# Optimization experiments

Measured on AMD Instinct MI355X. Metric: run time of the kernel, lower is better.

The kernel has to match this reference:

```python
import jax, jax.numpy as jnp
import numpy as np

N_NODES = 50000
N_EDGES = 800000
IN_FEATS = 128
H_FEATS = 128
NUM_CLASSES = 64


def _linear_params(key, fan_in, fan_out):
    kw, kb = jax.random.split(key)
    bound = 1.0 / np.sqrt(fan_in)
    W = jax.random.uniform(kw, (fan_out, fan_in), minval=-bound, maxval=bound, dtype=jnp.float32)
    b = jax.random.uniform(kb, (fan_out,), minval=-bound, maxval=bound, dtype=jnp.float32)
    return W, b


def setup_inputs() -> dict:
    key = jax.random.key(0)
    k_feat, k_src, k_dst, k1, k2, k3 = jax.random.split(key, 6)
    in_feat = jax.random.normal(k_feat, (N_NODES, IN_FEATS), dtype=jnp.float32)
    src = jax.random.randint(k_src, (N_EDGES,), 0, N_NODES, dtype=jnp.int32)
    dst = jax.random.randint(k_dst, (N_EDGES,), 0, N_NODES, dtype=jnp.int32)
    W1, b1 = _linear_params(k1, IN_FEATS, H_FEATS)
    W2, b2 = _linear_params(k2, H_FEATS, H_FEATS)
    W3, b3 = _linear_params(k3, H_FEATS, NUM_CLASSES)
    return {"in_feat": in_feat, "W1": W1, "b1": b1, "W2": W2, "b2": b2,
            "W3": W3, "b3": b3, "src": src, "dst": dst}


def reference(in_feat, W1, b1, W2, b2, W3, b3, src, dst):
    N = in_feat.shape[0]

    def gin_layer(x, W, b):
        # DGL GINConv with eps=0: (x + sum of in-neighbor messages) -> Linear
        agg = jax.ops.segment_sum(x[src], dst, num_segments=N)  # [N, d]
        return jax.nn.relu((x + agg) @ W.T + b)

    h = gin_layer(in_feat, W1, b1)
    h = gin_layer(h, W2, b2)
    h = gin_layer(h, W3, b3)
    return h
```

## Files before the change

kernel.cpp:

```cpp
#include <hip/hip_runtime.h>

typedef _Float16 half8 __attribute__((ext_vector_type(8)));
typedef _Float16 half2v __attribute__((ext_vector_type(2)));
typedef float floatx4 __attribute__((ext_vector_type(4)));
typedef unsigned int uintx4 __attribute__((ext_vector_type(4)));

union AB { uint4 u; half8 h; };
union H2 { unsigned int u; _Float16 h[2]; };
union H2P { unsigned int u; half2v h; };

#define CAPLOG 6
#define CAP 64

__global__ __launch_bounds__(256) void histA_init_k(
    const int* __restrict__ dst, int* __restrict__ histG, int E, int nbins,
    const float* __restrict__ W1, const float* __restrict__ W2, const float* __restrict__ W3,
    _Float16* __restrict__ W1h, _Float16* __restrict__ W2h, _Float16* __restrict__ W3h,
    _Float16* __restrict__ z1, _Float16* __restrict__ h1, _Float16* __restrict__ hZ,
    int n4w1, int n4w2, int n4w3, int zoff128, int zoff64) {
    int t = threadIdx.x;
    if (blockIdx.x < 256) {
        __shared__ int h[256];
        h[t] = 0;
        __syncthreads();
        int per = (E + 255) / 256;
        int beg = blockIdx.x * per;
        int end = min(E, beg + per);
        for (int e = beg + t; e < end; e += 256)
            atomicAdd(&h[dst[e] >> 8], 1);
        __syncthreads();
        for (int i = t; i < nbins; i += 256)
            histG[i * 256 + blockIdx.x] = h[i];
        return;
    }
    int i = (blockIdx.x - 256) * 256 + t;
    const float* X;
    _Float16* O;
    int j;
    if (i < n4w1) { X = W1; O = W1h; j = i; }
    else if (i < n4w1 + n4w2) { X = W2; O = W2h; j = i - n4w1; }
    else if (i < n4w1 + n4w2 + n4w3) { X = W3; O = W3h; j = i - n4w1 - n4w2; }
    else {
        int z = i - (n4w1 + n4w2 + n4w3);
        if (z < 16) ((uint4*)z1)[zoff128 + z] = make_uint4(0, 0, 0, 0);
        else if (z < 32) ((uint4*)h1)[zoff128 + (z - 16)] = make_uint4(0, 0, 0, 0);
        else if (z < 40) ((uint4*)hZ)[zoff64 + (z - 32)] = make_uint4(0, 0, 0, 0);
        return;
    }
    float4 v = reinterpret_cast<const float4*>(X)[j];
    union { uint2 u; _Float16 h[4]; } o;
    o.h[0] = (_Float16)v.x; o.h[1] = (_Float16)v.y;
    o.h[2] = (_Float16)v.z; o.h[3] = (_Float16)v.w;
    reinterpret_cast<uint2*>(O)[j] = o.u;
}

__global__ __launch_bounds__(1024) void scan1_k(const int* __restrict__ x,
                                                int* __restrict__ inc,
                                                int* __restrict__ partial, int n) {
    __shared__ int sd[1024];
    int t = threadIdx.x;
    int v = blockIdx.x * 1024 + t;
    sd[t] = (v < n) ? x[v] : 0;
    __syncthreads();
    for (int off = 1; off < 1024; off <<= 1) {
        int val = (t >= off) ? sd[t - off] : 0;
        __syncthreads();
        sd[t] += val;
        __syncthreads();
    }
    if (v < n) inc[v] = sd[t];
    if (t == 1023) partial[blockIdx.x] = sd[1023];
}

__global__ __launch_bounds__(256) void scatterB_k(const int* __restrict__ src,
                                                  const int* __restrict__ dst,
                                                  const int* __restrict__ inc,
                                                  const int* __restrict__ histG,
                                                  const int* __restrict__ partial, int nparts,
                                                  unsigned int* __restrict__ binned,
                                                  int E, int nbins) {
    __shared__ int cur[256];
    __shared__ int pp[64];
    int t = threadIdx.x, blk = blockIdx.x;
    if (t < 64) {
        int v = (t < nparts) ? partial[t] : 0;
        for (int off = 1; off < 64; off <<= 1) {
            int n = __shfl_up(v, off, 64);
            if (t >= off) v += n;
        }
        int ex = __shfl_up(v, 1, 64);
        if (t == 0) ex = 0;
        pp[t] = ex;
    }
    __syncthreads();
    for (int i = t; i < nbins; i += 256) {
        int idx = i * 256 + blk;
        cur[i] = inc[idx] + pp[idx >> 10] - histG[idx];
    }
    __syncthreads();
    int per = (E + 255) / 256;
    int beg = blk * per;
    int end = min(E, beg + per);
    for (int e = beg + t; e < end; e += 256) {
        int d = dst[e];
        int s = src[e];
        int pos = atomicAdd(&cur[d >> 8], 1);
        binned[pos] = ((unsigned int)(d & 255) << 16) | (unsigned int)s;
    }
}

__global__ __launch_bounds__(256) void binB_k(const unsigned int* __restrict__ binned,
                                              const int* __restrict__ inc,
                                              const int* __restrict__ histG,
                                              const int* __restrict__ partial, int nparts,
                                              unsigned short* __restrict__ col,
                                              int* __restrict__ cnt,
                                              int N, int E, int nbins) {
    __shared__ unsigned short lcol[256 * CAP];
    __shared__ int lcnt[256];
    __shared__ int pp[64];
    __shared__ int bounds[2];
    int t = threadIdx.x;
    int b = blockIdx.x;
    if (t < 64) {
        int v = (t < nparts) ? partial[t] : 0;
        for (int off = 1; off < 64; off <<= 1) {
            int n = __shfl_up(v, off, 64);
            if (t >= off) v += n;
        }
        int ex = __shfl_up(v, 1, 64);
        if (t == 0) ex = 0;
        pp[t] = ex;
    }
    unsigned int* lcol32 = (unsigned int*)lcol;
    for (int i = t; i < 256 * CAP / 2; i += 256) lcol32[i] = 0xFFFFFFFFu;
    lcnt[t] = 0;
    __syncthreads();
    if (t == 0) {
        int i0 = b * 256;
        bounds[0] = inc[i0] + pp[i0 >> 10] - histG[i0];
    } else if (t == 1) {
        if (b == nbins - 1) bounds[1] = E;
        else {
            int i1 = (b + 1) * 256;
            bounds[1] = inc[i1] + pp[i1 >> 10] - histG[i1];
        }
    }
    __syncthreads();
    int beg = bounds[0], end = bounds[1];
    for (int e = beg + t; e < end; e += 256) {
        unsigned int u = binned[e];
        int dl = u >> 16;
        int pos = atomicAdd(&lcnt[dl], 1);
        if (pos < CAP)
            lcol[(dl << CAPLOG) + ((pos & 3) << 4) + (pos >> 2)] = (unsigned short)(u & 0xFFFFu);
    }
    __syncthreads();
    int base = b << 8;
    int nodes = min(256, N - base);
    uint4* colg = (uint4*)(col + ((size_t)base << CAPLOG));
    const uint4* coll = (const uint4*)lcol;
    for (int i = t; i < nodes * 8; i += 256) colg[i] = coll[i];
    for (int i = t; i < nodes; i += 256) cnt[base + i] = lcnt[i];
}

__global__ __launch_bounds__(256) void gemm_z1_k(const float* __restrict__ X,
                                                 const _Float16* __restrict__ Wh,
                                                 _Float16* __restrict__ z1, int nnodes) {
    constexpr int WSTR = 136;
    __shared__ _Float16 Wl[128 * WSTR];

    const int t = threadIdx.x;
    for (int p = t; p < 128 * 16; p += 256) {
        int f = p >> 4;
        int kq = (p & 15) * 8;
        *reinterpret_cast<uint4*>(&Wl[f * WSTR + kq]) =
            *reinterpret_cast<const uint4*>(Wh + f * 128 + kq);
    }
    __syncthreads();

    const int wave = t >> 6;
    const int lane = t & 63;
    const int quad = lane >> 4;
    const int fcol = lane & 15;
    const int m_base = (blockIdx.x * 4 + wave) * 16;
    const int row = m_base + fcol;
    const bool rowok = row < nnodes;

    floatx4 acc[8];
#pragma unroll
    for (int ft = 0; ft < 8; ft++) acc[ft] = (floatx4){0.f, 0.f, 0.f, 0.f};

    const float* Xrow = X + (size_t)row * 128;
#pragma unroll
    for (int step = 0; step < 4; step++) {
        AB a;
        if (rowok) {
            float4 f0 = *reinterpret_cast<const float4*>(Xrow + step * 32 + quad * 8);
            float4 f1 = *reinterpret_cast<const float4*>(Xrow + step * 32 + quad * 8 + 4);
            a.h[0] = (_Float16)f0.x; a.h[1] = (_Float16)f0.y;
            a.h[2] = (_Float16)f0.z; a.h[3] = (_Float16)f0.w;
            a.h[4] = (_Float16)f1.x; a.h[5] = (_Float16)f1.y;
            a.h[6] = (_Float16)f1.z; a.h[7] = (_Float16)f1.w;
        } else a.u = make_uint4(0u, 0u, 0u, 0u);
#pragma unroll
        for (int ft = 0; ft < 8; ft++) {
            half8 b = *reinterpret_cast<const half8*>(
                &Wl[(ft * 16 + fcol) * WSTR + step * 32 + quad * 8]);
            acc[ft] = __builtin_amdgcn_mfma_f32_16x16x32_f16(a.h, b, acc[ft], 0, 0, 0);
        }
    }

#pragma unroll
    for (int ft = 0; ft < 8; ft++) {
        int f = ft * 16 + fcol;
#pragma unroll
        for (int r = 0; r < 4; r++) {
            int node = m_base + quad * 4 + r;
            if (node < nnodes)
                z1[(size_t)node * 128 + f] = (_Float16)acc[ft][r];
        }
    }
}

__global__ __launch_bounds__(256) void agg128_k(const _Float16* __restrict__ Z,
                                                const int* __restrict__ cnt,
                                                const unsigned short* __restrict__ col,
                                                const float* __restrict__ bias,
                                                _Float16* __restrict__ H, int nnodes) {
    int w = blockIdx.x * 4 + (threadIdx.x >> 6);
    int lane = threadIdx.x & 63;
    if (w >= nnodes) return;
    const int q = lane >> 4;
    const int c15 = lane & 15;
    const unsigned int* X32 = reinterpret_cast<const unsigned int*>(Z);
    int deg = cnt[w];
    if (deg > CAP) deg = CAP;
    int nb = (deg + 15) >> 4;
    const unsigned short* c = col + ((size_t)w << CAPLOG) + (q << 4);

    H2P a0[4], a1[4], a2[4], a3[4];
#pragma unroll
    for (int m = 0; m < 4; m++) { a0[m].u = 0u; a1[m].u = 0u; a2[m].u = 0u; a3[m].u = 0u; }

    for (int t = 0; t < nb; t++) {
        uint2 iw = *reinterpret_cast<const uint2*>(c + t * 4);
        int s0 = (int)(iw.x & 0xFFFFu); s0 = (s0 < nnodes) ? s0 : nnodes;
        int s1 = (int)(iw.x >> 16);     s1 = (s1 < nnodes) ? s1 : nnodes;
        int s2 = (int)(iw.y & 0xFFFFu); s2 = (s2 < nnodes) ? s2 : nnodes;
        int s3 = (int)(iw.y >> 16);     s3 = (s3 < nnodes) ? s3 : nnodes;
        uint4 v0 = *reinterpret_cast<const uint4*>(X32 + (size_t)s0 * 64 + c15 * 4);
        uint4 v1 = *reinterpret_cast<const uint4*>(X32 + (size_t)s1 * 64 + c15 * 4);
        uint4 v2 = *reinterpret_cast<const uint4*>(X32 + (size_t)s2 * 64 + c15 * 4);
        uint4 v3 = *reinterpret_cast<const uint4*>(X32 + (size_t)s3 * 64 + c15 * 4);
        H2P u;
        u.u = v0.x; a0[0].h += u.h;  u.u = v0.y; a0[1].h += u.h;
        u.u = v0.z; a0[2].h += u.h;  u.u = v0.w; a0[3].h += u.h;
        u.u = v1.x; a1[0].h += u.h;  u.u = v1.y; a1[1].h += u.h;
        u.u = v1.z; a1[2].h += u.h;  u.u = v1.w; a1[3].h += u.h;
        u.u = v2.x; a2[0].h += u.h;  u.u = v2.y; a2[1].h += u.h;
        u.u = v2.z; a2[2].h += u.h;  u.u = v2.w; a2[3].h += u.h;
        u.u = v3.x; a3[0].h += u.h;  u.u = v3.y; a3[1].h += u.h;
        u.u = v3.z; a3[2].h += u.h;  u.u = v3.w; a3[3].h += u.h;
    }
#pragma unroll
    for (int m = 0; m < 4; m++) {
        a0[m].h += a1[m].h;
        a2[m].h += a3[m].h;
        a0[m].h += a2[m].h;
    }
    float fs[8];
#pragma unroll
    for (int m = 0; m < 4; m++) {
        fs[2 * m] = (float)a0[m].h[0];
        fs[2 * m + 1] = (float)a0[m].h[1];
    }
#pragma unroll
    for (int m = 0; m < 8; m++) fs[m] += __shfl_xor(fs[m], 16, 64);
#pragma unroll
    for (int m = 0; m < 8; m++) fs[m] += __shfl_xor(fs[m], 32, 64);

    if (q == 0) {
        uint4 sv = *reinterpret_cast<const uint4*>(X32 + (size_t)w * 64 + c15 * 4);
        H2 x0, x1, x2, x3;
        x0.u = sv.x; x1.u = sv.y; x2.u = sv.z; x3.u = sv.w;
        float o[8];
        o[0] = (float)x0.h[0] + fs[0]; o[1] = (float)x0.h[1] + fs[1];
        o[2] = (float)x1.h[0] + fs[2]; o[3] = (float)x1.h[1] + fs[3];
        o[4] = (float)x2.h[0] + fs[4]; o[5] = (float)x2.h[1] + fs[5];
        o[6] = (float)x3.h[0] + fs[6]; o[7] = (float)x3.h[1] + fs[7];
        if (bias) {
            float4 b0 = *reinterpret_cast<const float4*>(bias + c15 * 8);
            float4 b1 = *reinterpret_cast<const float4*>(bias + c15 * 8 + 4);
            o[0] = fmaxf(o[0] + b0.x, 0.f); o[1] = fmaxf(o[1] + b0.y, 0.f);
            o[2] = fmaxf(o[2] + b0.z, 0.f); o[3] = fmaxf(o[3] + b0.w, 0.f);
            o[4] = fmaxf(o[4] + b1.x, 0.f); o[5] = fmaxf(o[5] + b1.y, 0.f);
            o[6] = fmaxf(o[6] + b1.z, 0.f); o[7] = fmaxf(o[7] + b1.w, 0.f);
        }
        H2 r0, r1, r2, r3;
        r0.h[0] = (_Float16)o[0]; r0.h[1] = (_Float16)o[1];
        r1.h[0] = (_Float16)o[2]; r1.h[1] = (_Float16)o[3];
        r2.h[0] = (_Float16)o[4]; r2.h[1] = (_Float16)o[5];
        r3.h[0] = (_Float16)o[6]; r3.h[1] = (_Float16)o[7];
        uintx4 ov;
        ov.x = r0.u; ov.y = r1.u; ov.z = r2.u; ov.w = r3.u;
        __builtin_nontemporal_store(
            ov, reinterpret_cast<uintx4*>(reinterpret_cast<unsigned int*>(H) +
                                          (size_t)w * 64 + c15 * 4));
    }
}

__global__ __launch_bounds__(256) void agg_final_k(const _Float16* __restrict__ Z,
                                                   const int* __restrict__ cnt,
                                                   const unsigned short* __restrict__ col,
                                                   const float* __restrict__ bias,
                                                   float* __restrict__ out, int nnodes) {
    int lane = threadIdx.x & 63;
    int sub = lane & 31;
    int node = blockIdx.x * 8 + (threadIdx.x >> 6) * 2 + (lane >> 5);
    if (node >= nnodes) return;
    const int q = sub >> 3;
    const int c7 = sub & 7;
    const unsigned int* Z32 = (const unsigned int*)Z;
    int deg = cnt[node];
    if (deg > CAP) deg = CAP;
    int nb = (deg + 15) >> 4;
    const unsigned short* c = col + ((size_t)node << CAPLOG) + (q << 4);

    H2P a0[4], a1[4], a2[4], a3[4];
#pragma unroll
    for (int m = 0; m < 4; m++) { a0[m].u = 0u; a1[m].u = 0u; a2[m].u = 0u; a3[m].u = 0u; }

    for (int t = 0; t < nb; t++) {
        uint2 iw = *reinterpret_cast<const uint2*>(c + t * 4);
        int s0 = (int)(iw.x & 0xFFFFu); s0 = (s0 < nnodes) ? s0 : nnodes;
        int s1 = (int)(iw.x >> 16);     s1 = (s1 < nnodes) ? s1 : nnodes;
        int s2 = (int)(iw.y & 0xFFFFu); s2 = (s2 < nnodes) ? s2 : nnodes;
        int s3 = (int)(iw.y >> 16);     s3 = (s3 < nnodes) ? s3 : nnodes;
        uint4 v0 = *reinterpret_cast<const uint4*>(Z32 + (size_t)s0 * 32 + c7 * 4);
        uint4 v1 = *reinterpret_cast<const uint4*>(Z32 + (size_t)s1 * 32 + c7 * 4);
        uint4 v2 = *reinterpret_cast<const uint4*>(Z32 + (size_t)s2 * 32 + c7 * 4);
        uint4 v3 = *reinterpret_cast<const uint4*>(Z32 + (size_t)s3 * 32 + c7 * 4);
        H2P u;
        u.u = v0.x; a0[0].h += u.h;  u.u = v0.y; a0[1].h += u.h;
        u.u = v0.z; a0[2].h += u.h;  u.u = v0.w; a0[3].h += u.h;
        u.u = v1.x; a1[0].h += u.h;  u.u = v1.y; a1[1].h += u.h;
        u.u = v1.z; a1[2].h += u.h;  u.u = v1.w; a1[3].h += u.h;
        u.u = v2.x; a2[0].h += u.h;  u.u = v2.y; a2[1].h += u.h;
        u.u = v2.z; a2[2].h += u.h;  u.u = v2.w; a2[3].h += u.h;
        u.u = v3.x; a3[0].h += u.h;  u.u = v3.y; a3[1].h += u.h;
        u.u = v3.z; a3[2].h += u.h;  u.u = v3.w; a3[3].h += u.h;
    }
#pragma unroll
    for (int m = 0; m < 4; m++) {
        a0[m].h += a1[m].h;
        a2[m].h += a3[m].h;
        a0[m].h += a2[m].h;
    }
    float fs[8];
#pragma unroll
    for (int m = 0; m < 4; m++) {
        fs[2 * m] = (float)a0[m].h[0];
        fs[2 * m + 1] = (float)a0[m].h[1];
    }
#pragma unroll
    for (int m = 0; m < 8; m++) fs[m] += __shfl_xor(fs[m], 8, 64);
#pragma unroll
    for (int m = 0; m < 8; m++) fs[m] += __shfl_xor(fs[m], 16, 64);

    if (q == 0) {
        uint4 sv = *reinterpret_cast<const uint4*>(Z32 + (size_t)node * 32 + c7 * 4);
        H2 x0, x1, x2, x3;
        x0.u = sv.x; x1.u = sv.y; x2.u = sv.z; x3.u = sv.w;
        float4 b0 = *reinterpret_cast<const float4*>(bias + c7 * 8);
        float4 b1 = *reinterpret_cast<const float4*>(bias + c7 * 8 + 4);
        float4 w0, w1;
        w0.x = fmaxf((float)x0.h[0] + fs[0] + b0.x, 0.f);
        w0.y = fmaxf((float)x0.h[1] + fs[1] + b0.y, 0.f);
        w0.z = fmaxf((float)x1.h[0] + fs[2] + b0.z, 0.f);
        w0.w = fmaxf((float)x1.h[1] + fs[3] + b0.w, 0.f);
        w1.x = fmaxf((float)x2.h[0] + fs[4] + b1.x, 0.f);
        w1.y = fmaxf((float)x2.h[1] + fs[5] + b1.y, 0.f);
        w1.z = fmaxf((float)x3.h[0] + fs[6] + b1.z, 0.f);
        w1.w = fmaxf((float)x3.h[1] + fs[7] + b1.w, 0.f);
        *reinterpret_cast<float4*>(out + (size_t)node * 64 + c7 * 8) = w0;
        *reinterpret_cast<float4*>(out + (size_t)node * 64 + c7 * 8 + 4) = w1;
    }
}

__global__ __launch_bounds__(256) void gemm23_k(const _Float16* __restrict__ Y,
                                                const _Float16* __restrict__ W2h,
                                                const float* __restrict__ b2,
                                                const _Float16* __restrict__ W3h,
                                                _Float16* __restrict__ hZ, int nnodes) {
    constexpr int WSTR = 136;
    __shared__ _Float16 Wl[128 * WSTR];
    __shared__ _Float16 Hl[64 * WSTR];
    __shared__ float Bl[128];

    const int t = threadIdx.x;
    for (int p = t; p < 128 * 16; p += 256) {
        int f = p >> 4;
        int kq = (p & 15) * 8;
        *reinterpret_cast<uint4*>(&Wl[f * WSTR + kq]) =
            *reinterpret_cast<const uint4*>(W2h + f * 128 + kq);
    }
    if (t < 128) Bl[t] = b2[t];
    __syncthreads();

    const int wave = t >> 6;
    const int lane = t & 63;
    const int quad = lane >> 4;
    const int fcol = lane & 15;
    const int m_base = (blockIdx.x * 4 + wave) * 16;
    const int row = m_base + fcol;
    const bool rowok = row < nnodes;

    floatx4 acc[8];
#pragma unroll
    for (int ft = 0; ft < 8; ft++) acc[ft] = (floatx4){0.f, 0.f, 0.f, 0.f};

    const uint4* Yrow = reinterpret_cast<const uint4*>(Y + (size_t)row * 128);
#pragma unroll
    for (int step = 0; step < 4; step++) {
        AB a;
        if (rowok) a.u = Yrow[step * 4 + quad];
        else       a.u = make_uint4(0u, 0u, 0u, 0u);
#pragma unroll
        for (int ft = 0; ft < 8; ft++) {
            half8 b = *reinterpret_cast<const half8*>(
                &Wl[(ft * 16 + fcol) * WSTR + step * 32 + quad * 8]);
            acc[ft] = __builtin_amdgcn_mfma_f32_16x16x32_f16(a.h, b, acc[ft], 0, 0, 0);
        }
    }

#pragma unroll
    for (int ft = 0; ft < 8; ft++) {
        int f = ft * 16 + fcol;
        float bv = Bl[f];
#pragma unroll
        for (int r = 0; r < 4; r++) {
            int nl = wave * 16 + quad * 4 + r;
            Hl[nl * WSTR + f] = (_Float16)fmaxf(acc[ft][r] + bv, 0.f);
        }
    }
    __syncthreads();

    for (int p = t; p < 64 * 16; p += 256) {
        int f = p >> 4;
        int kq = (p & 15) * 8;
        *reinterpret_cast<uint4*>(&Wl[f * WSTR + kq]) =
            *reinterpret_cast<const uint4*>(W3h + f * 128 + kq);
    }
    __syncthreads();

    floatx4 acc2[4];
#pragma unroll
    for (int ft = 0; ft < 4; ft++) acc2[ft] = (floatx4){0.f, 0.f, 0.f, 0.f};
#pragma unroll
    for (int step = 0; step < 4; step++) {
        AB a;
        a.h = *reinterpret_cast<const half8*>(
            &Hl[(wave * 16 + fcol) * WSTR + step * 32 + quad * 8]);
#pragma unroll
        for (int ft = 0; ft < 4; ft++) {
            half8 b = *reinterpret_cast<const half8*>(
                &Wl[(ft * 16 + fcol) * WSTR + step * 32 + quad * 8]);
            acc2[ft] = __builtin_amdgcn_mfma_f32_16x16x32_f16(a.h, b, acc2[ft], 0, 0, 0);
        }
    }
#pragma unroll
    for (int ft = 0; ft < 4; ft++) {
        int f = ft * 16 + fcol;
#pragma unroll
        for (int r = 0; r < 4; r++) {
            int node = m_base + quad * 4 + r;
            if (node < nnodes)
                hZ[(size_t)node * 64 + f] = (_Float16)acc2[ft][r];
        }
    }
}

extern "C" void kernel_launch(void* const* d_in, const int* in_sizes, int n_in,
                              void* d_out, int out_size, void* d_ws, size_t ws_size,
                              hipStream_t stream) {
    const float* in_feat = (const float*)d_in[0];
    const float* W1 = (const float*)d_in[1];
    const float* b1 = (const float*)d_in[2];
    const float* W2 = (const float*)d_in[3];
    const float* b2 = (const float*)d_in[4];
    const float* W3 = (const float*)d_in[5];
    const float* b3 = (const float*)d_in[6];
    const int* src = (const int*)d_in[7];
    const int* dst = (const int*)d_in[8];
    float* out = (float*)d_out;

    const int N = in_sizes[0] / 128;
    const int E = in_sizes[7];
    const int szW1 = in_sizes[1];
    const int szW2 = in_sizes[3];
    const int szW3 = in_sizes[5];
    const int nbins = (N + 255) >> 8;
    const int nhist = nbins * 256;

    char* p = (char*)d_ws;
    int* cnt = (int*)p;               p += (size_t)N * 4;
    unsigned short* col = (unsigned short*)p; p += (size_t)N * CAP * 2;
    int* histG = (int*)p;             p += (size_t)nhist * 4;
    int* incS = (int*)p;              p += (size_t)nhist * 4;
    int* partial = (int*)p;           p += 256;
    unsigned int* binned = (unsigned int*)p; p += (size_t)E * 4;
    _Float16* z1 = (_Float16*)p;      p += (size_t)(N + 1) * 128 * 2;
    _Float16* h1 = (_Float16*)p;      p += (size_t)(N + 1) * 128 * 2;
    _Float16* hB = (_Float16*)p;      p += (size_t)N * 128 * 2;
    _Float16* hZ = (_Float16*)p;      p += (size_t)(N + 1) * 64 * 2;
    _Float16* W1h = (_Float16*)p;     p += (size_t)szW1 * 2;
    _Float16* W2h = (_Float16*)p;     p += (size_t)szW2 * 2;
    _Float16* W3h = (_Float16*)p;     p += (size_t)szW3 * 2;

    const int nblk_scan = (nhist + 1023) / 1024;

    {
        int total = szW1 / 4 + szW2 / 4 + szW3 / 4 + 40;
        int iblk = (total + 255) / 256;
        histA_init_k<<<256 + iblk, 256, 0, stream>>>(dst, histG, E, nbins,
                                                     W1, W2, W3, W1h, W2h, W3h,
                                                     z1, h1, hZ,
                                                     szW1 / 4, szW2 / 4, szW3 / 4,
                                                     N * 16, N * 8);
    }
    scan1_k<<<nblk_scan, 1024, 0, stream>>>(histG, incS, partial, nhist);
    scatterB_k<<<256, 256, 0, stream>>>(src, dst, incS, histG, partial, nblk_scan,
                                        binned, E, nbins);
    binB_k<<<nbins, 256, 0, stream>>>(binned, incS, histG, partial, nblk_scan,
                                      col, cnt, N, E, nbins);

    const int nblk_agg = (N + 3) / 4;
    const int nblk_gemm = (N + 63) / 64;
    gemm_z1_k<<<nblk_gemm, 256, 0, stream>>>(in_feat, W1h, z1, N);
    agg128_k<<<nblk_agg, 256, 0, stream>>>(z1, cnt, col, b1, h1, N);
    agg128_k<<<nblk_agg, 256, 0, stream>>>(h1, cnt, col, nullptr, hB, N);
    gemm23_k<<<nblk_gemm, 256, 0, stream>>>(hB, W2h, b2, W3h, hZ, N);
    agg_final_k<<<(N + 7) / 8, 256, 0, stream>>>(hZ, cnt, col, b3, out, N);
}
```

Baseline: 223.1 us.

## Fuse layer-2 aggregation into GEMM23 and merge scatter with layer-1 GEMM

The layer-2 neighbor aggregation moves into the GEMM2/3 kernel, which gathers neighbor rows into shared memory before the MFMA. This removes the hB round trip and one launch. The edge scatter and the layer-1 GEMM now share one launch using block-index ranges, so the GEMM blocks can overlap with the atomic scatter. The fused kernel gathers with fewer threads per node (one wave handles 16 nodes serially), so it risks lower gather parallelism and latency hiding.

```diff
diff --git a/kernel.cpp b/kernel.cpp
--- a/kernel.cpp
+++ b/kernel.cpp
@@ -72,40 +72,98 @@
     if (t == 1023) partial[blockIdx.x] = sd[1023];
 }
 
-__global__ __launch_bounds__(256) void scatterB_k(const int* __restrict__ src,
-                                                  const int* __restrict__ dst,
-                                                  const int* __restrict__ inc,
-                                                  const int* __restrict__ histG,
-                                                  const int* __restrict__ partial, int nparts,
-                                                  unsigned int* __restrict__ binned,
-                                                  int E, int nbins) {
-    __shared__ int cur[256];
-    __shared__ int pp[64];
-    int t = threadIdx.x, blk = blockIdx.x;
-    if (t < 64) {
-        int v = (t < nparts) ? partial[t] : 0;
-        for (int off = 1; off < 64; off <<= 1) {
-            int n = __shfl_up(v, off, 64);
-            if (t >= off) v += n;
-        }
-        int ex = __shfl_up(v, 1, 64);
-        if (t == 0) ex = 0;
-        pp[t] = ex;
-    }
-    __syncthreads();
-    for (int i = t; i < nbins; i += 256) {
-        int idx = i * 256 + blk;
-        cur[i] = inc[idx] + pp[idx >> 10] - histG[idx];
-    }
-    __syncthreads();
-    int per = (E + 255) / 256;
-    int beg = blk * per;
-    int end = min(E, beg + per);
-    for (int e = beg + t; e < end; e += 256) {
-        int d = dst[e];
-        int s = src[e];
-        int pos = atomicAdd(&cur[d >> 8], 1);
-        binned[pos] = ((unsigned int)(d & 255) << 16) | (unsigned int)s;
+__global__ __launch_bounds__(256) void scatgemm_k(
+    const int* __restrict__ src, const int* __restrict__ dst,
+    const int* __restrict__ inc, const int* __restrict__ histG,
+    const int* __restrict__ partial, int nparts,
+    unsigned int* __restrict__ binned, int E, int nbins,
+    const float* __restrict__ X, const _Float16* __restrict__ Wh,
+    _Float16* __restrict__ z1, int nnodes) {
+    constexpr int WSTR = 136;
+    __shared__ _Float16 Wl[128 * WSTR];
+
+    const int t = threadIdx.x;
+    if (blockIdx.x < 256) {
+        int* cur = (int*)Wl;
+        int* pp = cur + 256;
+        int blk = blockIdx.x;
+        if (t < 64) {
+            int v = (t < nparts) ? partial[t] : 0;
+            for (int off = 1; off < 64; off <<= 1) {
+                int n = __shfl_up(v, off, 64);
+                if (t >= off) v += n;
+            }
+            int ex = __shfl_up(v, 1, 64);
+            if (t == 0) ex = 0;
+            pp[t] = ex;
+        }
+        __syncthreads();
+        for (int i = t; i < nbins; i += 256) {
+            int idx = i * 256 + blk;
+            cur[i] = inc[idx] + pp[idx >> 10] - histG[idx];
+        }
+        __syncthreads();
+        int per = (E + 255) / 256;
+        int beg = blk * per;
+        int end = min(E, beg + per);
+        for (int e = beg + t; e < end; e += 256) {
+            int d = dst[e];
+            int s = src[e];
+            int pos = atomicAdd(&cur[d >> 8], 1);
+            binned[pos] = ((unsigned int)(d & 255) << 16) | (unsigned int)s;
+        }
+        return;
+    }
+
+    for (int p = t; p < 128 * 16; p += 256) {
+        int f = p >> 4;
+        int kq = (p & 15) * 8;
+        *reinterpret_cast<uint4*>(&Wl[f * WSTR + kq]) =
+            *reinterpret_cast<const uint4*>(Wh + f * 128 + kq);
+    }
+    __syncthreads();
+
+    const int wave = t >> 6;
+    const int lane = t & 63;
+    const int quad = lane >> 4;
+    const int fcol = lane & 15;
+    const int m_base = ((blockIdx.x - 256) * 4 + wave) * 16;
+    const int row = m_base + fcol;
+    const bool rowok = row < nnodes;
+
+    floatx4 acc[8];
+#pragma unroll
+    for (int ft = 0; ft < 8; ft++) acc[ft] = (floatx4){0.f, 0.f, 0.f, 0.f};
+
+    const float* Xrow = X + (size_t)row * 128;
+#pragma unroll
+    for (int step = 0; step < 4; step++) {
+        AB a;
+        if (rowok) {
+            float4 f0 = *reinterpret_cast<const float4*>(Xrow + step * 32 + quad * 8);
+            float4 f1 = *reinterpret_cast<const float4*>(Xrow + step * 32 + quad * 8 + 4);
+            a.h[0] = (_Float16)f0.x; a.h[1] = (_Float16)f0.y;
+            a.h[2] = (_Float16)f0.z; a.h[3] = (_Float16)f0.w;
+            a.h[4] = (_Float16)f1.x; a.h[5] = (_Float16)f1.y;
+            a.h[6] = (_Float16)f1.z; a.h[7] = (_Float16)f1.w;
+        } else a.u = make_uint4(0u, 0u, 0u, 0u);
+#pragma unroll
+        for (int ft = 0; ft < 8; ft++) {
+            half8 b = *reinterpret_cast<const half8*>(
+                &Wl[(ft * 16 + fcol) * WSTR + step * 32 + quad * 8]);
+            acc[ft] = __builtin_amdgcn_mfma_f32_16x16x32_f16(a.h, b, acc[ft], 0, 0, 0);
+        }
+    }
+
+#pragma unroll
+    for (int ft = 0; ft < 8; ft++) {
+        int f = ft * 16 + fcol;
+#pragma unroll
+        for (int r = 0; r < 4; r++) {
+            int node = m_base + quad * 4 + r;
+            if (node < nnodes)
+                z1[(size_t)node * 128 + f] = (_Float16)acc[ft][r];
+        }
     }
 }
 
@@ -162,65 +220,6 @@
     const uint4* coll = (const uint4*)lcol;
     for (int i = t; i < nodes * 8; i += 256) colg[i] = coll[i];
     for (int i = t; i < nodes; i += 256) cnt[base + i] = lcnt[i];
-}
-
-__global__ __launch_bounds__(256) void gemm_z1_k(const float* __restrict__ X,
-                                                 const _Float16* __restrict__ Wh,
-                                                 _Float16* __restrict__ z1, int nnodes) {
-    constexpr int WSTR = 136;
-    __shared__ _Float16 Wl[128 * WSTR];
-
-    const int t = threadIdx.x;
-    for (int p = t; p < 128 * 16; p += 256) {
-        int f = p >> 4;
-        int kq = (p & 15) * 8;
-        *reinterpret_cast<uint4*>(&Wl[f * WSTR + kq]) =
-            *reinterpret_cast<const uint4*>(Wh + f * 128 + kq);
-    }
-    __syncthreads();
-
-    const int wave = t >> 6;
-    const int lane = t & 63;
-    const int quad = lane >> 4;
-    const int fcol = lane & 15;
-    const int m_base = (blockIdx.x * 4 + wave) * 16;
-    const int row = m_base + fcol;
-    const bool rowok = row < nnodes;
-
-    floatx4 acc[8];
-#pragma unroll
-    for (int ft = 0; ft < 8; ft++) acc[ft] = (floatx4){0.f, 0.f, 0.f, 0.f};
-
-    const float* Xrow = X + (size_t)row * 128;
-#pragma unroll
-    for (int step = 0; step < 4; step++) {
-        AB a;
-        if (rowok) {
-            float4 f0 = *reinterpret_cast<const float4*>(Xrow + step * 32 + quad * 8);
-            float4 f1 = *reinterpret_cast<const float4*>(Xrow + step * 32 + quad * 8 + 4);
-            a.h[0] = (_Float16)f0.x; a.h[1] = (_Float16)f0.y;
-            a.h[2] = (_Float16)f0.z; a.h[3] = (_Float16)f0.w;
-            a.h[4] = (_Float16)f1.x; a.h[5] = (_Float16)f1.y;
-            a.h[6] = (_Float16)f1.z; a.h[7] = (_Float16)f1.w;
-        } else a.u = make_uint4(0u, 0u, 0u, 0u);
-#pragma unroll
-        for (int ft = 0; ft < 8; ft++) {
-            half8 b = *reinterpret_cast<const half8*>(
-                &Wl[(ft * 16 + fcol) * WSTR + step * 32 + quad * 8]);
-            acc[ft] = __builtin_amdgcn_mfma_f32_16x16x32_f16(a.h, b, acc[ft], 0, 0, 0);
-        }
-    }
-
-#pragma unroll
-    for (int ft = 0; ft < 8; ft++) {
-        int f = ft * 16 + fcol;
-#pragma unroll
-        for (int r = 0; r < 4; r++) {
-            int node = m_base + quad * 4 + r;
-            if (node < nnodes)
-                z1[(size_t)node * 128 + f] = (_Float16)acc[ft][r];
-        }
-    }
 }
 
 __global__ __launch_bounds__(256) void agg128_k(const _Float16* __restrict__ Z,
@@ -284,19 +283,17 @@
         uint4 sv = *reinterpret_cast<const uint4*>(X32 + (size_t)w * 64 + c15 * 4);
         H2 x0, x1, x2, x3;
         x0.u = sv.x; x1.u = sv.y; x2.u = sv.z; x3.u = sv.w;
+        float4 b0 = *reinterpret_cast<const float4*>(bias + c15 * 8);
+        float4 b1 = *reinterpret_cast<const float4*>(bias + c15 * 8 + 4);
         float o[8];
-        o[0] = (float)x0.h[0] + fs[0]; o[1] = (float)x0.h[1] + fs[1];
-        o[2] = (float)x1.h[0] + fs[2]; o[3] = (float)x1.h[1] + fs[3];
-        o[4] = (float)x2.h[0] + fs[4]; o[5] = (float)x2.h[1] + fs[5];
-        o[6] = (float)x3.h[0] + fs[6]; o[7] = (float)x3.h[1] + fs[7];
-        if (bias) {
-            float4 b0 = *reinterpret_cast<const float4*>(bias + c15 * 8);
-            float4 b1 = *reinterpret_cast<const float4*>(bias + c15 * 8 + 4);
-            o[0] = fmaxf(o[0] + b0.x, 0.f); o[1] = fmaxf(o[1] + b0.y, 0.f);
-            o[2] = fmaxf(o[2] + b0.z, 0.f); o[3] = fmaxf(o[3] + b0.w, 0.f);
-            o[4] = fmaxf(o[4] + b1.x, 0.f); o[5] = fmaxf(o[5] + b1.y, 0.f);
-            o[6] = fmaxf(o[6] + b1.z, 0.f); o[7] = fmaxf(o[7] + b1.w, 0.f);
-        }
+        o[0] = fmaxf((float)x0.h[0] + fs[0] + b0.x, 0.f);
+        o[1] = fmaxf((float)x0.h[1] + fs[1] + b0.y, 0.f);
+        o[2] = fmaxf((float)x1.h[0] + fs[2] + b0.z, 0.f);
+        o[3] = fmaxf((float)x1.h[1] + fs[3] + b0.w, 0.f);
+        o[4] = fmaxf((float)x2.h[0] + fs[4] + b1.x, 0.f);
+        o[5] = fmaxf((float)x2.h[1] + fs[5] + b1.y, 0.f);
+        o[6] = fmaxf((float)x3.h[0] + fs[6] + b1.z, 0.f);
+        o[7] = fmaxf((float)x3.h[1] + fs[7] + b1.w, 0.f);
         H2 r0, r1, r2, r3;
         r0.h[0] = (_Float16)o[0]; r0.h[1] = (_Float16)o[1];
         r1.h[0] = (_Float16)o[2]; r1.h[1] = (_Float16)o[3];
@@ -388,11 +385,13 @@
     }
 }
 
-__global__ __launch_bounds__(256) void gemm23_k(const _Float16* __restrict__ Y,
-                                                const _Float16* __restrict__ W2h,
-                                                const float* __restrict__ b2,
-                                                const _Float16* __restrict__ W3h,
-                                                _Float16* __restrict__ hZ, int nnodes) {
+__global__ __launch_bounds__(256) void gemm23f_k(const _Float16* __restrict__ Y,
+                                                 const int* __restrict__ cnt,
+                                                 const unsigned short* __restrict__ col,
+                                                 const _Float16* __restrict__ W2h,
+                                                 const float* __restrict__ b2,
+                                                 const _Float16* __restrict__ W3h,
+                                                 _Float16* __restrict__ hZ, int nnodes) {
     constexpr int WSTR = 136;
     __shared__ _Float16 Wl[128 * WSTR];
     __shared__ _Float16 Hl[64 * WSTR];
@@ -406,26 +405,99 @@
             *reinterpret_cast<const uint4*>(W2h + f * 128 + kq);
     }
     if (t < 128) Bl[t] = b2[t];
-    __syncthreads();
 
     const int wave = t >> 6;
     const int lane = t & 63;
     const int quad = lane >> 4;
     const int fcol = lane & 15;
     const int m_base = (blockIdx.x * 4 + wave) * 16;
-    const int row = m_base + fcol;
-    const bool rowok = row < nnodes;
+    const unsigned int* X32 = reinterpret_cast<const unsigned int*>(Y);
+
+    for (int i = 0; i < 16; i++) {
+        int node = m_base + i;
+        unsigned int* Hrow = reinterpret_cast<unsigned int*>(&Hl[(wave * 16 + i) * WSTR]);
+        if (node >= nnodes) {
+            if (quad == 0) {
+                uintx4 zz; zz.x = 0u; zz.y = 0u; zz.z = 0u; zz.w = 0u;
+                *reinterpret_cast<uintx4*>(Hrow + fcol * 4) = zz;
+            }
+            continue;
+        }
+        int deg = cnt[node];
+        if (deg > CAP) deg = CAP;
+        int nb = (deg + 15) >> 4;
+        const unsigned short* c = col + ((size_t)node << CAPLOG) + (quad << 4);
+
+        H2P a0[4], a1[4], a2[4], a3[4];
+#pragma unroll
+        for (int m = 0; m < 4; m++) { a0[m].u = 0u; a1[m].u = 0u; a2[m].u = 0u; a3[m].u = 0u; }
+
+        for (int tt = 0; tt < nb; tt++) {
+            uint2 iw = *reinterpret_cast<const uint2*>(c + tt * 4);
+            int s0 = (int)(iw.x & 0xFFFFu); s0 = (s0 < nnodes) ? s0 : nnodes;
+            int s1 = (int)(iw.x >> 16);     s1 = (s1 < nnodes) ? s1 : nnodes;
+            int s2 = (int)(iw.y & 0xFFFFu); s2 = (s2 < nnodes) ? s2 : nnodes;
+            int s3 = (int)(iw.y >> 16);     s3 = (s3 < nnodes) ? s3 : nnodes;
+            uint4 v0 = *reinterpret_cast<const uint4*>(X32 + (size_t)s0 * 64 + fcol * 4);
+            uint4 v1 = *reinterpret_cast<const uint4*>(X32 + (size_t)s1 * 64 + fcol * 4);
+            uint4 v2 = *reinterpret_cast<const uint4*>(X32 + (size_t)s2 * 64 + fcol * 4);
+            uint4 v3 = *reinterpret_cast<const uint4*>(X32 + (size_t)s3 * 64 + fcol * 4);
+            H2P u;
+            u.u = v0.x; a0[0].h += u.h;  u.u = v0.y; a0[1].h += u.h;
+            u.u = v0.z; a0[2].h += u.h;  u.u = v0.w; a0[3].h += u.h;
+            u.u = v1.x; a1[0].h += u.h;  u.u = v1.y; a1[1].h += u.h;
+            u.u = v1.z; a1[2].h += u.h;  u.u = v1.w; a1[3].h += u.h;
+            u.u = v2.x; a2[0].h += u.h;  u.u = v2.y; a2[1].h += u.h;
+            u.u = v2.z; a2[2].h += u.h;  u.u = v2.w; a2[3].h += u.h;
+            u.u = v3.x; a3[0].h += u.h;  u.u = v3.y; a3[1].h += u.h;
+            u.u = v3.z; a3[2].h += u.h;  u.u = v3.w; a3[3].h += u.h;
+        }
+#pragma unroll
+        for (int m = 0; m < 4; m++) {
+            a0[m].h += a1[m].h;
+            a2[m].h += a3[m].h;
+            a0[m].h += a2[m].h;
+        }
+        float fs[8];
+#pragma unroll
+        for (int m = 0; m < 4; m++) {
+            fs[2 * m] = (float)a0[m].h[0];
+            fs[2 * m + 1] = (float)a0[m].h[1];
+        }
+#pragma unroll
+        for (int m = 0; m < 8; m++) fs[m] += __shfl_xor(fs[m], 16, 64);
+#pragma unroll
+        for (int m = 0; m < 8; m++) fs[m] += __shfl_xor(fs[m], 32, 64);
+
+        if (quad == 0) {
+            uint4 sv = *reinterpret_cast<const uint4*>(X32 + (size_t)node * 64 + fcol * 4);
+            H2 x0, x1, x2, x3;
+            x0.u = sv.x; x1.u = sv.y; x2.u = sv.z; x3.u = sv.w;
+            H2 r0, r1, r2, r3;
+            r0.h[0] = (_Float16)((float)x0.h[0] + fs[0]);
+            r0.h[1] = (_Float16)((float)x0.h[1] + fs[1]);
+            r1.h[0] = (_Float16)((float)x1.h[0] + fs[2]);
+            r1.h[1] = (_Float16)((float)x1.h[1] + fs[3]);
+            r2.h[0] = (_Float16)((float)x2.h[0] + fs[4]);
+            r2.h[1] = (_Float16)((float)x2.h[1] + fs[5]);
+            r3.h[0] = (_Float16)((float)x3.h[0] + fs[6]);
+            r3.h[1] = (_Float16)((float)x3.h[1] + fs[7]);
+            uintx4 ov;
+            ov.x = r0.u; ov.y = r1.u; ov.z = r2.u; ov.w = r3.u;
+            *reinterpret_cast<uintx4*>(Hrow + fcol * 4) = ov;
+        }
+    }
+    __syncthreads();
 
     floatx4 acc[8];
 #pragma unroll
     for (int ft = 0; ft < 8; ft++) acc[ft] = (floatx4){0.f, 0.f, 0.f, 0.f};
 
-    const uint4* Yrow = reinterpret_cast<const uint4*>(Y + (size_t)row * 128);
 #pragma unroll
     for (int step = 0; step < 4; step++) {
         AB a;
-        if (rowok) a.u = Yrow[step * 4 + quad];
-        else       a.u = make_uint4(0u, 0u, 0u, 0u);
+        a.h = *reinterpret_cast<const half8*>(
+            &Hl[(wave * 16 + fcol) * WSTR + step * 32 + quad * 8]);
 #pragma unroll
         for (int ft = 0; ft < 8; ft++) {
             half8 b = *reinterpret_cast<const half8*>(
@@ -512,13 +584,14 @@
     unsigned int* binned = (unsigned int*)p; p += (size_t)E * 4;
     _Float16* z1 = (_Float16*)p;      p += (size_t)(N + 1) * 128 * 2;
     _Float16* h1 = (_Float16*)p;      p += (size_t)(N + 1) * 128 * 2;
-    _Float16* hB = (_Float16*)p;      p += (size_t)N * 128 * 2;
     _Float16* hZ = (_Float16*)p;      p += (size_t)(N + 1) * 64 * 2;
     _Float16* W1h = (_Float16*)p;     p += (size_t)szW1 * 2;
     _Float16* W2h = (_Float16*)p;     p += (size_t)szW2 * 2;
     _Float16* W3h = (_Float16*)p;     p += (size_t)szW3 * 2;
 
     const int nblk_scan = (nhist + 1023) / 1024;
+    const int nblk_gemm = (N + 63) / 64;
+    const int nblk_agg = (N + 3) / 4;
 
     {
         int total = szW1 / 4 + szW2 / 4 + szW3 / 4 + 40;
@@ -530,16 +603,12 @@
                                                      N * 16, N * 8);
     }
     scan1_k<<<nblk_scan, 1024, 0, stream>>>(histG, incS, partial, nhist);
-    scatterB_k<<<256, 256, 0, stream>>>(src, dst, incS, histG, partial, nblk_scan,
-                                        binned, E, nbins);
+    scatgemm_k<<<256 + nblk_gemm, 256, 0, stream>>>(src, dst, incS, histG, partial,
+                                                    nblk_scan, binned, E, nbins,
+                                                    in_feat, W1h, z1, N);
     binB_k<<<nbins, 256, 0, stream>>>(binned, incS, histG, partial, nblk_scan,
                                       col, cnt, N, E, nbins);
-
-    const int nblk_agg = (N + 3) / 4;
-    const int nblk_gemm = (N + 63) / 64;
-    gemm_z1_k<<<nblk_gemm, 256, 0, stream>>>(in_feat, W1h, z1, N);
     agg128_k<<<nblk_agg, 256, 0, stream>>>(z1, cnt, col, b1, h1, N);
-    agg128_k<<<nblk_agg, 256, 0, stream>>>(h1, cnt, col, nullptr, hB, N);
-    gemm23_k<<<nblk_gemm, 256, 0, stream>>>(hB, W2h, b2, W3h, hZ, N);
+    gemm23f_k<<<nblk_gemm, 256, 0, stream>>>(h1, cnt, col, W2h, b2, W3h, hZ, N);
     agg_final_k<<<(N + 7) / 8, 256, 0, stream>>>(hZ, cnt, col, b3, out, N);
 }
```

Result: slower. 245.3 us (+9.9%).

## Merge CSR build and first GEMM into one cooperative kernel with grid syncs

Applied to the files above, without the earlier changes.

Replaces the histogram, scan, scatter, bin and first-layer GEMM launches with a single 256-block cooperative kernel that separates phases with grid.sync. The scan is restructured into a per-bin 256-wide scan plus a single-block scan of bin totals, replacing the 1024-wide scan and the repeated partial-prefix recomputation. The goal is to remove the launch gaps between five small kernels. In exchange, the GEMM now runs on only 256 persistent blocks, each looping over tiles, which may cut its parallelism and its latency hiding, and the grid syncs add their own cost.

```diff
diff --git a/kernel.cpp b/kernel.cpp
--- a/kernel.cpp
+++ b/kernel.cpp
@@ -1,4 +1,7 @@
 #include <hip/hip_runtime.h>
+#include <hip/hip_cooperative_groups.h>
+
+namespace cg = cooperative_groups;
 
 typedef _Float16 half8 __attribute__((ext_vector_type(8)));
 typedef _Float16 half2v __attribute__((ext_vector_type(2)));
@@ -12,213 +15,191 @@
 #define CAPLOG 6
 #define CAP 64
 
-__global__ __launch_bounds__(256) void histA_init_k(
-    const int* __restrict__ dst, int* __restrict__ histG, int E, int nbins,
+__global__ __launch_bounds__(256) void coop_k(
+    const int* __restrict__ src, const int* __restrict__ dst,
+    int* __restrict__ histG, int* __restrict__ Pex, int* __restrict__ T, int* __restrict__ B,
+    unsigned int* __restrict__ binned,
+    unsigned short* __restrict__ col, int* __restrict__ cnt,
+    int E, int N, int nbins,
     const float* __restrict__ W1, const float* __restrict__ W2, const float* __restrict__ W3,
     _Float16* __restrict__ W1h, _Float16* __restrict__ W2h, _Float16* __restrict__ W3h,
     _Float16* __restrict__ z1, _Float16* __restrict__ h1, _Float16* __restrict__ hZ,
-    int n4w1, int n4w2, int n4w3, int zoff128, int zoff64) {
-    int t = threadIdx.x;
-    if (blockIdx.x < 256) {
-        __shared__ int h[256];
+    int n4w1, int n4w2, int n4w3,
+    const float* __restrict__ X) {
+    __shared__ __align__(16) char smem[34816];
+    cg::grid_group grid = cg::this_grid();
+    const int t = threadIdx.x;
+    const int blk = blockIdx.x;
+
+    {
+        int* h = (int*)smem;
         h[t] = 0;
         __syncthreads();
+        int gid = blk * 256 + t;
+        int total = n4w1 + n4w2 + n4w3 + 40;
+        if (gid < total) {
+            const float* Xw = nullptr;
+            _Float16* O = nullptr;
+            int j = 0;
+            if (gid < n4w1) { Xw = W1; O = W1h; j = gid; }
+            else if (gid < n4w1 + n4w2) { Xw = W2; O = W2h; j = gid - n4w1; }
+            else if (gid < n4w1 + n4w2 + n4w3) { Xw = W3; O = W3h; j = gid - n4w1 - n4w2; }
+            else {
+                int z = gid - (n4w1 + n4w2 + n4w3);
+                if (z < 16) ((uint4*)z1)[(size_t)N * 16 + z] = make_uint4(0, 0, 0, 0);
+                else if (z < 32) ((uint4*)h1)[(size_t)N * 16 + (z - 16)] = make_uint4(0, 0, 0, 0);
+                else ((uint4*)hZ)[(size_t)N * 8 + (z - 32)] = make_uint4(0, 0, 0, 0);
+            }
+            if (Xw) {
+                float4 v = reinterpret_cast<const float4*>(Xw)[j];
+                union { uint2 u; _Float16 hh[4]; } o;
+                o.hh[0] = (_Float16)v.x; o.hh[1] = (_Float16)v.y;
+                o.hh[2] = (_Float16)v.z; o.hh[3] = (_Float16)v.w;
+                reinterpret_cast<uint2*>(O)[j] = o.u;
+            }
+        }
         int per = (E + 255) / 256;
-        int beg = blockIdx.x * per;
+        int beg = blk * per;
         int end = min(E, beg + per);
         for (int e = beg + t; e < end; e += 256)
             atomicAdd(&h[dst[e] >> 8], 1);
         __syncthreads();
         for (int i = t; i < nbins; i += 256)
-            histG[i * 256 + blockIdx.x] = h[i];
-        return;
-    }
-    int i = (blockIdx.x - 256) * 256 + t;
-    const float* X;
-    _Float16* O;
-    int j;
-    if (i < n4w1) { X = W1; O = W1h; j = i; }
-    else if (i < n4w1 + n4w2) { X = W2; O = W2h; j = i - n4w1; }
-    else if (i < n4w1 + n4w2 + n4w3) { X = W3; O = W3h; j = i - n4w1 - n4w2; }
-    else {
-        int z = i - (n4w1 + n4w2 + n4w3);
-        if (z < 16) ((uint4*)z1)[zoff128 + z] = make_uint4(0, 0, 0, 0);
-        else if (z < 32) ((uint4*)h1)[zoff128 + (z - 16)] = make_uint4(0, 0, 0, 0);
-        else if (z < 40) ((uint4*)hZ)[zoff64 + (z - 32)] = make_uint4(0, 0, 0, 0);
-        return;
-    }
-    float4 v = reinterpret_cast<const float4*>(X)[j];
-    union { uint2 u; _Float16 h[4]; } o;
-    o.h[0] = (_Float16)v.x; o.h[1] = (_Float16)v.y;
-    o.h[2] = (_Float16)v.z; o.h[3] = (_Float16)v.w;
-    reinterpret_cast<uint2*>(O)[j] = o.u;
-}
-
-__global__ __launch_bounds__(1024) void scan1_k(const int* __restrict__ x,
-                                                int* __restrict__ inc,
-                                                int* __restrict__ partial, int n) {
-    __shared__ int sd[1024];
-    int t = threadIdx.x;
-    int v = blockIdx.x * 1024 + t;
-    sd[t] = (v < n) ? x[v] : 0;
-    __syncthreads();
-    for (int off = 1; off < 1024; off <<= 1) {
-        int val = (t >= off) ? sd[t - off] : 0;
-        __syncthreads();
-        sd[t] += val;
-        __syncthreads();
-    }
-    if (v < n) inc[v] = sd[t];
-    if (t == 1023) partial[blockIdx.x] = sd[1023];
-}
-
-__global__ __launch_bounds__(256) void scatterB_k(const int* __restrict__ src,
-                                                  const int* __restrict__ dst,
-                                                  const int* __restrict__ inc,
-                                                  const int* __restrict__ histG,
-                                                  const int* __restrict__ partial, int nparts,
-                                                  unsigned int* __restrict__ binned,
-                                                  int E, int nbins) {
-    __shared__ int cur[256];
-    __shared__ int pp[64];
-    int t = threadIdx.x, blk = blockIdx.x;
-    if (t < 64) {
-        int v = (t < nparts) ? partial[t] : 0;
-        for (int off = 1; off < 64; off <<= 1) {
-            int n = __shfl_up(v, off, 64);
-            if (t >= off) v += n;
-        }
-        int ex = __shfl_up(v, 1, 64);
-        if (t == 0) ex = 0;
-        pp[t] = ex;
-    }
-    __syncthreads();
-    for (int i = t; i < nbins; i += 256) {
-        int idx = i * 256 + blk;
-        cur[i] = inc[idx] + pp[idx >> 10] - histG[idx];
-    }
-    __syncthreads();
-    int per = (E + 255) / 256;
-    int beg = blk * per;
-    int end = min(E, beg + per);
-    for (int e = beg + t; e < end; e += 256) {
-        int d = dst[e];
-        int s = src[e];
-        int pos = atomicAdd(&cur[d >> 8], 1);
-        binned[pos] = ((unsigned int)(d & 255) << 16) | (unsigned int)s;
-    }
-}
-
-__global__ __launch_bounds__(256) void binB_k(const unsigned int* __restrict__ binned,
-                                              const int* __restrict__ inc,
-                                              const int* __restrict__ histG,
-                                              const int* __restrict__ partial, int nparts,
-                                              unsigned short* __restrict__ col,
-                                              int* __restrict__ cnt,
-                                              int N, int E, int nbins) {
-    __shared__ unsigned short lcol[256 * CAP];
-    __shared__ int lcnt[256];
-    __shared__ int pp[64];
-    __shared__ int bounds[2];
-    int t = threadIdx.x;
-    int b = blockIdx.x;
-    if (t < 64) {
-        int v = (t < nparts) ? partial[t] : 0;
-        for (int off = 1; off < 64; off <<= 1) {
-            int n = __shfl_up(v, off, 64);
-            if (t >= off) v += n;
-        }
-        int ex = __shfl_up(v, 1, 64);
-        if (t == 0) ex = 0;
-        pp[t] = ex;
-    }
-    unsigned int* lcol32 = (unsigned int*)lcol;
-    for (int i = t; i < 256 * CAP / 2; i += 256) lcol32[i] = 0xFFFFFFFFu;
-    lcnt[t] = 0;
-    __syncthreads();
-    if (t == 0) {
-        int i0 = b * 256;
-        bounds[0] = inc[i0] + pp[i0 >> 10] - histG[i0];
-    } else if (t == 1) {
-        if (b == nbins - 1) bounds[1] = E;
-        else {
-            int i1 = (b + 1) * 256;
-            bounds[1] = inc[i1] + pp[i1 >> 10] - histG[i1];
-        }
-    }
-    __syncthreads();
-    int beg = bounds[0], end = bounds[1];
-    for (int e = beg + t; e < end; e += 256) {
-        unsigned int u = binned[e];
-        int dl = u >> 16;
-        int pos = atomicAdd(&lcnt[dl], 1);
-        if (pos < CAP)
-            lcol[(dl << CAPLOG) + ((pos & 3) << 4) + (pos >> 2)] = (unsigned short)(u & 0xFFFFu);
-    }
-    __syncthreads();
-    int base = b << 8;
-    int nodes = min(256, N - base);
-    uint4* colg = (uint4*)(col + ((size_t)base << CAPLOG));
-    const uint4* coll = (const uint4*)lcol;
-    for (int i = t; i < nodes * 8; i += 256) colg[i] = coll[i];
-    for (int i = t; i < nodes; i += 256) cnt[base + i] = lcnt[i];
-}
-
-__global__ __launch_bounds__(256) void gemm_z1_k(const float* __restrict__ X,
-                                                 const _Float16* __restrict__ Wh,
-                                                 _Float16* __restrict__ z1, int nnodes) {
-    constexpr int WSTR = 136;
-    __shared__ _Float16 Wl[128 * WSTR];
-
-    const int t = threadIdx.x;
-    for (int p = t; p < 128 * 16; p += 256) {
-        int f = p >> 4;
-        int kq = (p & 15) * 8;
-        *reinterpret_cast<uint4*>(&Wl[f * WSTR + kq]) =
-            *reinterpret_cast<const uint4*>(Wh + f * 128 + kq);
-    }
-    __syncthreads();
-
-    const int wave = t >> 6;
-    const int lane = t & 63;
-    const int quad = lane >> 4;
-    const int fcol = lane & 15;
-    const int m_base = (blockIdx.x * 4 + wave) * 16;
-    const int row = m_base + fcol;
-    const bool rowok = row < nnodes;
-
-    floatx4 acc[8];
-#pragma unroll
-    for (int ft = 0; ft < 8; ft++) acc[ft] = (floatx4){0.f, 0.f, 0.f, 0.f};
-
-    const float* Xrow = X + (size_t)row * 128;
-#pragma unroll
-    for (int step = 0; step < 4; step++) {
-        AB a;
-        if (rowok) {
-            float4 f0 = *reinterpret_cast<const float4*>(Xrow + step * 32 + quad * 8);
-            float4 f1 = *reinterpret_cast<const float4*>(Xrow + step * 32 + quad * 8 + 4);
-            a.h[0] = (_Float16)f0.x; a.h[1] = (_Float16)f0.y;
-            a.h[2] = (_Float16)f0.z; a.h[3] = (_Float16)f0.w;
-            a.h[4] = (_Float16)f1.x; a.h[5] = (_Float16)f1.y;
-            a.h[6] = (_Float16)f1.z; a.h[7] = (_Float16)f1.w;
-        } else a.u = make_uint4(0u, 0u, 0u, 0u);
-#pragma unroll
-        for (int ft = 0; ft < 8; ft++) {
-            half8 b = *reinterpret_cast<const half8*>(
-                &Wl[(ft * 16 + fcol) * WSTR + step * 32 + quad * 8]);
-            acc[ft] = __builtin_amdgcn_mfma_f32_16x16x32_f16(a.h, b, acc[ft], 0, 0, 0);
-        }
-    }
-
-#pragma unroll
-    for (int ft = 0; ft < 8; ft++) {
-        int f = ft * 16 + fcol;
-#pragma unroll
-        for (int r = 0; r < 4; r++) {
-            int node = m_base + quad * 4 + r;
-            if (node < nnodes)
-                z1[(size_t)node * 128 + f] = (_Float16)acc[ft][r];
+            histG[i * 256 + blk] = h[i];
+    }
+    grid.sync();
+
+    if (blk < nbins) {
+        int* sd = (int*)smem;
+        int v = histG[blk * 256 + t];
+        sd[t] = v;
+        __syncthreads();
+        for (int off = 1; off < 256; off <<= 1) {
+            int val = (t >= off) ? sd[t - off] : 0;
+            __syncthreads();
+            sd[t] += val;
+            __syncthreads();
+        }
+        Pex[blk * 256 + t] = sd[t] - v;
+        if (t == 255) T[blk] = sd[255];
+    }
+    grid.sync();
+
+    if (blk == 0) {
+        int* sd = (int*)smem;
+        int v = (t < nbins) ? T[t] : 0;
+        sd[t] = v;
+        __syncthreads();
+        for (int off = 1; off < 256; off <<= 1) {
+            int val = (t >= off) ? sd[t - off] : 0;
+            __syncthreads();
+            sd[t] += val;
+            __syncthreads();
+        }
+        if (t < nbins) B[t] = sd[t] - v;
+    }
+    grid.sync();
+
+    {
+        int* cur = (int*)smem;
+        for (int i = t; i < nbins; i += 256)
+            cur[i] = B[i] + Pex[i * 256 + blk];
+        __syncthreads();
+        int per = (E + 255) / 256;
+        int beg = blk * per;
+        int end = min(E, beg + per);
+        for (int e = beg + t; e < end; e += 256) {
+            int d = dst[e];
+            int s = src[e];
+            int pos = atomicAdd(&cur[d >> 8], 1);
+            binned[pos] = ((unsigned int)(d & 255) << 16) | (unsigned int)s;
+        }
+    }
+    grid.sync();
+
+    if (blk < nbins) {
+        unsigned short* lcol = (unsigned short*)smem;
+        int* lcnt = (int*)(smem + 32768);
+        unsigned int* lcol32 = (unsigned int*)lcol;
+        for (int i = t; i < 256 * CAP / 2; i += 256) lcol32[i] = 0xFFFFFFFFu;
+        lcnt[t] = 0;
+        __syncthreads();
+        int beg = B[blk];
+        int end = (blk == nbins - 1) ? E : B[blk + 1];
+        for (int e = beg + t; e < end; e += 256) {
+            unsigned int u = binned[e];
+            int dl = u >> 16;
+            int pos = atomicAdd(&lcnt[dl], 1);
+            if (pos < CAP)
+                lcol[(dl << CAPLOG) + ((pos & 3) << 4) + (pos >> 2)] =
+                    (unsigned short)(u & 0xFFFFu);
+        }
+        __syncthreads();
+        int base = blk << 8;
+        int nodes = min(256, N - base);
+        uint4* colg = (uint4*)(col + ((size_t)base << CAPLOG));
+        const uint4* coll = (const uint4*)lcol;
+        for (int i = t; i < nodes * 8; i += 256) colg[i] = coll[i];
+        for (int i = t; i < nodes; i += 256) cnt[base + i] = lcnt[i];
+    }
+    grid.sync();
+
+    {
+        constexpr int WSTR = 136;
+        _Float16* Wl = (_Float16*)smem;
+        for (int p = t; p < 128 * 16; p += 256) {
+            int f = p >> 4;
+            int kq = (p & 15) * 8;
+            *reinterpret_cast<uint4*>(&Wl[f * WSTR + kq]) =
+                *reinterpret_cast<const uint4*>(W1h + f * 128 + kq);
+        }
+        __syncthreads();
+
+        const int wave = t >> 6;
+        const int lane = t & 63;
+        const int quad = lane >> 4;
+        const int fcol = lane & 15;
+        const int ntiles = (N + 63) >> 6;
+
+        for (int tile = blk; tile < ntiles; tile += 256) {
+            const int m_base = tile * 64 + wave * 16;
+            const int row = m_base + fcol;
+            const bool rowok = row < N;
+
+            floatx4 acc[8];
+#pragma unroll
+            for (int ft = 0; ft < 8; ft++) acc[ft] = (floatx4){0.f, 0.f, 0.f, 0.f};
+
+            const float* Xrow = X + (size_t)row * 128;
+#pragma unroll
+            for (int step = 0; step < 4; step++) {
+                AB a;
+                if (rowok) {
+                    float4 f0 = *reinterpret_cast<const float4*>(Xrow + step * 32 + quad * 8);
+                    float4 f1 = *reinterpret_cast<const float4*>(Xrow + step * 32 + quad * 8 + 4);
+                    a.h[0] = (_Float16)f0.x; a.h[1] = (_Float16)f0.y;
+                    a.h[2] = (_Float16)f0.z; a.h[3] = (_Float16)f0.w;
+                    a.h[4] = (_Float16)f1.x; a.h[5] = (_Float16)f1.y;
+                    a.h[6] = (_Float16)f1.z; a.h[7] = (_Float16)f1.w;
+                } else a.u = make_uint4(0u, 0u, 0u, 0u);
+#pragma unroll
+                for (int ft = 0; ft < 8; ft++) {
+                    half8 b = *reinterpret_cast<const half8*>(
+                        &Wl[(ft * 16 + fcol) * WSTR + step * 32 + quad * 8]);
+                    acc[ft] = __builtin_amdgcn_mfma_f32_16x16x32_f16(a.h, b, acc[ft], 0, 0, 0);
+                }
+            }
+
+#pragma unroll
+            for (int ft = 0; ft < 8; ft++) {
+                int f = ft * 16 + fcol;
+#pragma unroll
+                for (int r = 0; r < 4; r++) {
+                    int node = m_base + quad * 4 + r;
+                    if (node < N)
+                        z1[(size_t)node * 128 + f] = (_Float16)acc[ft][r];
+                }
+            }
         }
     }
 }
@@ -507,8 +488,9 @@
     int* cnt = (int*)p;               p += (size_t)N * 4;
     unsigned short* col = (unsigned short*)p; p += (size_t)N * CAP * 2;
     int* histG = (int*)p;             p += (size_t)nhist * 4;
-    int* incS = (int*)p;              p += (size_t)nhist * 4;
-    int* partial = (int*)p;           p += 256;
+    int* Pex = (int*)p;               p += (size_t)nhist * 4;
+    int* T = (int*)p;                 p += 1024;
+    int* B = (int*)p;                 p += 1024;
     unsigned int* binned = (unsigned int*)p; p += (size_t)E * 4;
     _Float16* z1 = (_Float16*)p;      p += (size_t)(N + 1) * 128 * 2;
     _Float16* h1 = (_Float16*)p;      p += (size_t)(N + 1) * 128 * 2;
@@ -518,26 +500,23 @@
     _Float16* W2h = (_Float16*)p;     p += (size_t)szW2 * 2;
     _Float16* W3h = (_Float16*)p;     p += (size_t)szW3 * 2;
 
-    const int nblk_scan = (nhist + 1023) / 1024;
-
     {
-        int total = szW1 / 4 + szW2 / 4 + szW3 / 4 + 40;
-        int iblk = (total + 255) / 256;
-        histA_init_k<<<256 + iblk, 256, 0, stream>>>(dst, histG, E, nbins,
-                                                     W1, W2, W3, W1h, W2h, W3h,
-                                                     z1, h1, hZ,
-                                                     szW1 / 4, szW2 / 4, szW3 / 4,
-                                                     N * 16, N * 8);
-    }
-    scan1_k<<<nblk_scan, 1024, 0, stream>>>(histG, incS, partial, nhist);
-    scatterB_k<<<256, 256, 0, stream>>>(src, dst, incS, histG, partial, nblk_scan,
-                                        binned, E, nbins);
-    binB_k<<<nbins, 256, 0, stream>>>(binned, incS, histG, partial, nblk_scan,
-                                      col, cnt, N, E, nbins);
+        int E_ = E, N_ = N, nbins_ = nbins;
+        int n4w1 = szW1 / 4, n4w2 = szW2 / 4, n4w3 = szW3 / 4;
+        const int* src_ = src; const int* dst_ = dst;
+        const float* W1_ = W1; const float* W2_ = W2; const float* W3_ = W3;
+        const float* X_ = in_feat;
+        void* cargs[] = {
+            (void*)&src_, (void*)&dst_, (void*)&histG, (void*)&Pex, (void*)&T, (void*)&B,
+            (void*)&binned, (void*)&col, (void*)&cnt, (void*)&E_, (void*)&N_, (void*)&nbins_,
+            (void*)&W1_, (void*)&W2_, (void*)&W3_, (void*)&W1h, (void*)&W2h, (void*)&W3h,
+            (void*)&z1, (void*)&h1, (void*)&hZ, (void*)&n4w1, (void*)&n4w2, (void*)&n4w3,
+            (void*)&X_};
+        hipLaunchCooperativeKernel(coop_k, dim3(256), dim3(256), cargs, 0, stream);
+    }
 
     const int nblk_agg = (N + 3) / 4;
     const int nblk_gemm = (N + 63) / 64;
-    gemm_z1_k<<<nblk_gemm, 256, 0, stream>>>(in_feat, W1h, z1, N);
     agg128_k<<<nblk_agg, 256, 0, stream>>>(z1, cnt, col, b1, h1, N);
     agg128_k<<<nblk_agg, 256, 0, stream>>>(h1, cnt, col, nullptr, hB, N);
     gemm23_k<<<nblk_gemm, 256, 0, stream>>>(hB, W2h, b2, W3h, hZ, N);
```

After: 398.8 us. 78.7% more time.
